# Kernel optimization log

Measured on AMD Instinct MI355X. Metric: run time of the kernel, lower is better.

## Reference

```python
import jax, jax.numpy as jnp
import numpy as np

UNITS = 768
OUT_STEPS = 64
INPUT_DIM = 96


def setup_inputs() -> dict:
    key = jax.random.key(0)
    ks = jax.random.split(key, 7)
    B, T = 2048, 24
    s_ih = 1.0 / np.sqrt(UNITS)
    inputs = jax.random.normal(ks[0], (B, T, INPUT_DIM), dtype=jnp.float32)
    # PyTorch LSTMCell params: weight_ih [4U, I], weight_hh [4U, U], biases [4U]
    W_ih = jax.random.uniform(ks[1], (4 * UNITS, INPUT_DIM), minval=-s_ih, maxval=s_ih, dtype=jnp.float32)
    W_hh = jax.random.uniform(ks[2], (4 * UNITS, UNITS), minval=-s_ih, maxval=s_ih, dtype=jnp.float32)
    b_ih = jax.random.uniform(ks[3], (4 * UNITS,), minval=-s_ih, maxval=s_ih, dtype=jnp.float32)
    b_hh = jax.random.uniform(ks[4], (4 * UNITS,), minval=-s_ih, maxval=s_ih, dtype=jnp.float32)
    # Dense: Linear(units, input_dim)
    s_d = 1.0 / np.sqrt(UNITS)
    W_d = jax.random.uniform(ks[5], (INPUT_DIM, UNITS), minval=-s_d, maxval=s_d, dtype=jnp.float32)
    b_d = jax.random.uniform(ks[6], (INPUT_DIM,), minval=-s_d, maxval=s_d, dtype=jnp.float32)
    return {"inputs": inputs, "W_ih": W_ih, "W_hh": W_hh, "b_ih": b_ih, "b_hh": b_hh, "W_d": W_d, "b_d": b_d}


def _lstm_cell(x, h, c, W_ih, W_hh, b_ih, b_hh):
    # gates: [B, 4U], PyTorch gate order i, f, g, o
    gates = x @ W_ih.T + b_ih + h @ W_hh.T + b_hh
    i, f, g, o = jnp.split(gates, 4, axis=-1)
    i = jax.nn.sigmoid(i)
    f = jax.nn.sigmoid(f)
    g = jnp.tanh(g)
    o = jax.nn.sigmoid(o)
    c_new = f * c + i * g
    h_new = o * jnp.tanh(c_new)
    return h_new, c_new


def reference(inputs, W_ih, W_hh, b_ih, b_hh, W_d, b_d):
    B = inputs.shape[0]
    h0 = jnp.zeros((B, UNITS), dtype=inputs.dtype)
    c0 = jnp.zeros((B, UNITS), dtype=inputs.dtype)
    # warmup: feed last timestep
    x0 = inputs[:, -1, :]
    h, c = _lstm_cell(x0, h0, c0, W_ih, W_hh, b_ih, b_hh)
    pred0 = h @ W_d.T + b_d

    def step(carry, _):
        pred, h, c = carry
        h2, c2 = _lstm_cell(pred, h, c, W_ih, W_hh, b_ih, b_hh)
        pred2 = h2 @ W_d.T + b_d
        return (pred2, h2, c2), pred2

    _, preds_rest = jax.lax.scan(step, (pred0, h, c), None, length=OUT_STEPS - 1)
    # preds_rest: [out_steps-1, B, I] -> stack with pred0 along time axis 1
    preds = jnp.concatenate([pred0[None], preds_rest], axis=0)  # [out_steps, B, I]
    return jnp.transpose(preds, (1, 0, 2))  # [B, out_steps, I]
```

## Files before the change

kernel.cpp:

```cpp
#include <hip/hip_runtime.h>
#include <hip/hip_bf16.h>
#include <stdint.h>

typedef __hip_bfloat16 bf16_t;
typedef __attribute__((ext_vector_type(4))) float f32x4;
typedef __attribute__((ext_vector_type(8))) short s16x8;

#define UNITS 768
#define NCOLS 3072
#define NPRED 96
#define MROWS 2048

__device__ __forceinline__ float sigf(float x) {
    return __builtin_amdgcn_rcpf(1.f + __expf(-x));
}
__device__ __forceinline__ float tanh_fast(float x) {
    return 1.f - 2.f * __builtin_amdgcn_rcpf(1.f + __expf(2.f * x));
}


__global__ void prep_b0(const float* __restrict__ W_ih, bf16_t* __restrict__ B0T) {
    int idx = blockIdx.x * 256 + threadIdx.x;
    if (idx >= NCOLS * 96) return;
    int c = idx / 96, k = idx % 96;
    int u = ((c >> 6) << 4) + (c & 15);
    int g = (c >> 4) & 3;
    B0T[idx] = (bf16_t)W_ih[(g * UNITS + u) * 96 + k];
}

__global__ void prep_x0(const float* __restrict__ inputs, bf16_t* __restrict__ x0) {
    int idx = blockIdx.x * 256 + threadIdx.x;
    int j = idx & 7;
    int l = (idx >> 3) & 63;
    int fg = idx >> 9;
    int kf = fg % 3;
    int mf = fg / 3;
    int m = mf * 16 + (l & 15);
    int k = kf * 32 + (l >> 4) * 8 + j;
    x0[idx] = (bf16_t)inputs[(m * 24 + 23) * 96 + k];
}

__global__ void prep_bias(const float* __restrict__ b_ih, const float* __restrict__ b_hh,
                          const float* __restrict__ W_ih, const float* __restrict__ b_d,
                          float* __restrict__ b0_r, float* __restrict__ beff_r) {
    int c = blockIdx.x * 256 + threadIdx.x;
    if (c >= NCOLS) return;
    int u = ((c >> 6) << 4) + (c & 15);
    int g = (c >> 4) & 3;
    int r = g * UNITS + u;
    float v = b_ih[r] + b_hh[r];
    float acc = 0.f;
    for (int j = 0; j < 96; ++j) acc += W_ih[r * 96 + j] * b_d[j];
    b0_r[c] = v;
    beff_r[c] = v + acc;
}

__global__ void prep_beff2(const float* __restrict__ W_hh, const float* __restrict__ W_ih,
                           const float* __restrict__ W_d, bf16_t* __restrict__ BeffT) {
    __shared__ float sWih[64][96];
    __shared__ float sWd[96][64];
    const int c0 = blockIdx.x * 64, k0 = blockIdx.y * 64;
    const int tid = threadIdx.x;
    for (int i = tid; i < 64 * 96; i += 256) {
        int cc = i / 96, j = i % 96;
        int c = c0 + cc;
        int u = ((c >> 6) << 4) + (c & 15);
        int g = (c >> 4) & 3;
        sWih[cc][j] = W_ih[(g * UNITS + u) * 96 + j];
    }
    for (int i = tid; i < 96 * 64; i += 256) {
        int j = i / 64, kk = i % 64;
        sWd[j][kk] = W_d[j * UNITS + k0 + kk];
    }
    __syncthreads();
    const int kk = tid & 63;
    const int cc0 = (tid >> 6) * 16;
    for (int cc = cc0; cc < cc0 + 16; ++cc) {
        float acc = 0.f;
#pragma unroll 12
        for (int j = 0; j < 96; ++j) acc += sWih[cc][j] * sWd[j][kk];
        int c = c0 + cc;
        int u = ((c >> 6) << 4) + (c & 15);
        int g = (c >> 4) & 3;
        int r = g * UNITS + u;
        BeffT[(size_t)c * UNITS + k0 + kk] = (bf16_t)(W_hh[(size_t)r * UNITS + k0 + kk] + acc);
    }
}

__global__ void prep_wdt(const float* __restrict__ W_d, bf16_t* __restrict__ BeffT) {
    int idx = blockIdx.x * 256 + threadIdx.x;
    int c = idx / UNITS, k = idx % UNITS;
    float v = (c < NPRED) ? W_d[c * UNITS + k] : 0.f;
    BeffT[(size_t)(NCOLS + c) * UNITS + k] = (bf16_t)v;
}

__global__ void prep_swz(const bf16_t* __restrict__ src, bf16_t* __restrict__ dst,
                         int Knk, int K, int total) {
    int idx = blockIdx.x * 256 + threadIdx.x;
    if (idx >= total) return;
    int j = idx & 7;
    int l = (idx >> 3) & 63;
    int fg = idx >> 9;
    int f = fg & 3;
    int rest = fg >> 2;
    int kf = rest % Knk;
    int nw = rest / Knk;
    int c = (nw >> 1) * 128 + (nw & 1) * 64 + f * 16 + (l & 15);
    int k = kf * 32 + (l >> 4) * 8 + j;
    dst[idx] = src[(size_t)c * K + k];
}

__global__ __launch_bounds__(256, 2)
void step_kernel(const bf16_t* __restrict__ A,
                 const bf16_t* __restrict__ B,
                 const float* __restrict__ bias_r,
                 const float* __restrict__ b_d,
                 float* __restrict__ c_state,
                 bf16_t* __restrict__ h_out,
                 float* __restrict__ out,
                 int Knk, int nt_off, int t, int is_first)
{
    const int tid = threadIdx.x;
    const int wave = tid >> 6;
    const int lane = tid & 63;
    const int wr = wave >> 1, wc = wave & 1;
    const int l15 = lane & 15, l4 = lane >> 4;

    const int per = gridDim.x >> 3;
    const int g = (blockIdx.x & 7) * per + (blockIdx.x >> 3);
    const int nt = nt_off + (g >> 4);
    const int mt = g & 15;
    const int n0 = nt * 128;
    const bool is_pred = (nt >= 24);

    const bf16_t* Ab[4];
#pragma unroll
    for (int i = 0; i < 4; ++i)
        Ab[i] = A + ((size_t)((mt * 8 + wr * 4 + i) * Knk) * 64 + lane) * 8;
    const bf16_t* Bb[4];
#pragma unroll
    for (int f = 0; f < 4; ++f)
        Bb[f] = B + ((size_t)((nt * 2 + wc) * Knk * 4 + f) * 64 + lane) * 8;

    const int u = nt * 32 + wc * 16 + l15;
    const int slot = nt * 16 + mt;
    float* cbase = c_state + (((size_t)slot * 4 + wave) * 64 + lane) * 16;
    f32x4 cold4[4];
    float bi[4];
#pragma unroll
    for (int q = 0; q < 4; ++q) cold4[q] = f32x4{0.f, 0.f, 0.f, 0.f};
    if (!is_pred) {
        if (!is_first) {
#pragma unroll
            for (int q = 0; q < 4; ++q) cold4[q] = *(const f32x4*)(cbase + q * 4);
        }
#pragma unroll
        for (int f = 0; f < 4; ++f) bi[f] = bias_r[n0 + wc * 64 + f * 16 + l15];
    } else {
#pragma unroll
        for (int f = 0; f < 4; ++f) {
            int j = wc * 64 + f * 16 + l15;
            bi[f] = (j < NPRED) ? b_d[j] : 0.f;
        }
    }

    f32x4 acc[4][4];
#pragma unroll
    for (int i = 0; i < 4; ++i)
#pragma unroll
        for (int j = 0; j < 4; ++j) acc[i][j] = f32x4{0.f, 0.f, 0.f, 0.f};

    s16x8 afr[3][4], bfr[3][4];
    const int nk = Knk;

#define LOADK(BUF, KT) do {                                                          \
        _Pragma("unroll")                                                            \
        for (int _i = 0; _i < 4; ++_i)                                               \
            afr[BUF][_i] = *(const s16x8*)(Ab[_i] + (size_t)(KT) * 512);             \
        _Pragma("unroll")                                                            \
        for (int _f = 0; _f < 4; ++_f)                                               \
            bfr[BUF][_f] = *(const s16x8*)(Bb[_f] + (size_t)(KT) * 2048);            \
    } while (0)
#define MF(BUF) do {                                                                 \
        _Pragma("unroll")                                                            \
        for (int _i = 0; _i < 4; ++_i)                                               \
            _Pragma("unroll")                                                        \
            for (int _j = 0; _j < 4; ++_j)                                           \
                acc[_i][_j] = __builtin_amdgcn_mfma_f32_16x16x32_bf16(               \
                    afr[BUF][_i], bfr[BUF][_j], acc[_i][_j], 0, 0, 0);               \
    } while (0)

    LOADK(0, 0);
    LOADK(1, 1);
    const int nk3 = nk / 3;
    for (int b3 = 0; b3 < nk3; ++b3) {
        const int kt = b3 * 3;
        if (kt + 2 < nk) LOADK(2, kt + 2);
        MF(0);
        if (kt + 3 < nk) LOADK(0, kt + 3);
        MF(1);
        if (kt + 4 < nk) LOADK(1, kt + 4);
        MF(2);
    }
#undef LOADK
#undef MF

    if (!is_pred) {
        const int kq = wc * 2 + (l15 >> 3);
        const int jj = l15 & 7;
        f32x4 cnew4[4];
#pragma unroll
        for (int i = 0; i < 4; ++i) {
            const int mf = mt * 8 + wr * 4 + i;
            bf16_t* hb = h_out + (size_t)(mf * 24 + nt) * 512;
#pragma unroll
            for (int r = 0; r < 4; ++r) {
                float gi = acc[i][0][r] + bi[0];
                float gf = acc[i][1][r] + bi[1];
                float gg = acc[i][2][r] + bi[2];
                float go = acc[i][3][r] + bi[3];
                float si = sigf(gi);
                float sf = sigf(gf);
                float tg = tanh_fast(gg);
                float so = sigf(go);
                float cn = sf * cold4[i][r] + si * tg;
                cnew4[i][r] = cn;
                int lp = (l4 * 4 + r) | (kq << 4);
                hb[lp * 8 + jj] = (bf16_t)(so * tanh_fast(cn));
            }
        }
#pragma unroll
        for (int q = 0; q < 4; ++q) *(f32x4*)(cbase + q * 4) = cnew4[q];
    } else {
#pragma unroll
        for (int f = 0; f < 4; ++f) {
            int j = wc * 64 + f * 16 + l15;
            if (j < NPRED) {
#pragma unroll
                for (int i = 0; i < 4; ++i)
#pragma unroll
                    for (int r = 0; r < 4; ++r) {
                        int row = mt * 128 + wr * 64 + i * 16 + l4 * 4 + r;
                        out[((size_t)row * 64 + (t - 1)) * NPRED + j] = acc[i][f][r] + bi[f];
                    }
            }
        }
    }
}

extern "C" void kernel_launch(void* const* d_in, const int* in_sizes, int n_in,
                              void* d_out, int out_size, void* d_ws, size_t ws_size,
                              hipStream_t stream)
{
    const float* inputs = (const float*)d_in[0];
    const float* W_ih   = (const float*)d_in[1];
    const float* W_hh   = (const float*)d_in[2];
    const float* b_ih   = (const float*)d_in[3];
    const float* b_hh   = (const float*)d_in[4];
    const float* W_d    = (const float*)d_in[5];
    const float* b_d    = (const float*)d_in[6];
    float* out = (float*)d_out;

    char* ws = (char*)d_ws;
    size_t off = 0;
    auto alloc = [&](size_t bytes) -> char* {
        char* p = ws + off;
        off = (off + bytes + 255) & ~(size_t)255;
        return p;
    };
    bf16_t* B0T   = (bf16_t*)alloc((size_t)NCOLS * 96 * 2);
    bf16_t* B0s   = (bf16_t*)alloc((size_t)NCOLS * 96 * 2);
    bf16_t* BeffT = (bf16_t*)alloc((size_t)3200 * UNITS * 2);
    bf16_t* Bs    = (bf16_t*)alloc((size_t)3200 * UNITS * 2);
    bf16_t* x0s   = (bf16_t*)alloc((size_t)MROWS * 96 * 2);
    bf16_t* h0    = (bf16_t*)alloc((size_t)MROWS * UNITS * 2);
    bf16_t* h1    = (bf16_t*)alloc((size_t)MROWS * UNITS * 2);
    float*  cst   = (float*)alloc((size_t)384 * 4 * 64 * 16 * 4);
    float*  b0r   = (float*)alloc(NCOLS * 4);
    float*  beffr = (float*)alloc(NCOLS * 4);

    prep_b0   <<<(NCOLS * 96 + 255) / 256, 256, 0, stream>>>(W_ih, B0T);
    prep_swz  <<<(NCOLS * 96 + 255) / 256, 256, 0, stream>>>(B0T, B0s, 3, 96, NCOLS * 96);
    prep_x0   <<<(MROWS * 96) / 256, 256, 0, stream>>>(inputs, x0s);
    prep_bias <<<(NCOLS + 255) / 256, 256, 0, stream>>>(b_ih, b_hh, W_ih, b_d, b0r, beffr);
    prep_beff2<<<dim3(48, 12), 256, 0, stream>>>(W_hh, W_ih, W_d, BeffT);
    prep_wdt  <<<(128 * UNITS) / 256, 256, 0, stream>>>(W_d, BeffT);
    prep_swz  <<<(3200 * UNITS + 255) / 256, 256, 0, stream>>>(BeffT, Bs, 24, UNITS, 3200 * UNITS);

    bf16_t* h[2] = {h0, h1};

    step_kernel<<<384, 256, 0, stream>>>(x0s, B0s, b0r, b_d, cst, h[1], out, 3, 0, 0, 1);
    for (int n = 1; n < 64; ++n)
        step_kernel<<<400, 256, 0, stream>>>(h[n & 1], Bs, beffr, b_d, cst,
                                             h[(n + 1) & 1], out, 24, 0, n, 0);
    step_kernel<<<16, 256, 0, stream>>>(h[0], Bs, beffr, b_d, cst, h[1], out,
                                        24, 24, 64, 0);
    (void)ws_size; (void)in_sizes; (void)n_in; (void)out_size;
}
```

Measured before the change: 1.349 ms.

## Fuse all LSTM steps into one persistent cooperative kernel with grid barriers

```diff
diff --git a/kernel.cpp b/kernel.cpp
--- a/kernel.cpp
+++ b/kernel.cpp
@@ -18,6 +18,10 @@
     return 1.f - 2.f * __builtin_amdgcn_rcpf(1.f + __expf(2.f * x));
 }
 
+
+__global__ void prep_zero(unsigned int* c) {
+    if (threadIdx.x < 64) c[threadIdx.x] = 0u;
+}
 
 __global__ void prep_b0(const float* __restrict__ W_ih, bf16_t* __restrict__ B0T) {
     int idx = blockIdx.x * 256 + threadIdx.x;
@@ -108,6 +112,202 @@
     int c = (nw >> 1) * 128 + (nw & 1) * 64 + f * 16 + (l & 15);
     int k = kf * 32 + (l >> 4) * 8 + j;
     dst[idx] = src[(size_t)c * K + k];
+}
+
+__global__ __launch_bounds__(256, 1)
+void persist_kernel(const bf16_t* __restrict__ x0s,
+                    const bf16_t* __restrict__ B0s,
+                    const bf16_t* __restrict__ Bs,
+                    const float* __restrict__ b0r,
+                    const float* __restrict__ beffr,
+                    const float* __restrict__ b_d,
+                    bf16_t* __restrict__ h0,
+                    bf16_t* __restrict__ h1,
+                    float* __restrict__ out,
+                    unsigned int* __restrict__ ctrs)
+{
+    const int tid = threadIdx.x;
+    const int wave = tid >> 6;
+    const int lane = tid & 63;
+    const int l15 = lane & 15, l4 = lane >> 4;
+
+    __shared__ int s_id;
+
+    if (tid == 0) {
+        unsigned int x;
+        asm volatile("s_getreg_b32 %0, hwreg(20, 0, 32)" : "=s"(x));
+        x &= 7u;
+        unsigned int r = atomicAdd(&ctrs[x], 1u);
+        __threadfence();
+        unsigned int gq = atomicAdd(&ctrs[8], 1u);
+        while (__hip_atomic_load(&ctrs[8], __ATOMIC_RELAXED, __HIP_MEMORY_SCOPE_AGENT) < 256u)
+            __builtin_amdgcn_s_sleep(2);
+        __threadfence();
+        unsigned int mn = 0xffffffffu;
+        for (int y = 0; y < 8; ++y) {
+            unsigned int v = __hip_atomic_load(&ctrs[y], __ATOMIC_RELAXED, __HIP_MEMORY_SCOPE_AGENT);
+            mn = (v < mn) ? v : mn;
+        }
+        int id;
+        if (mn >= 25u) id = (r < 25u) ? (int)(x * 25u + r) : -1;
+        else           id = (gq < 200u) ? (int)gq : -1;
+        s_id = id;
+    }
+    __syncthreads();
+    const int id = s_id;
+    const bool active = (id >= 0);
+    const int mt = active ? (id & 7) : 0;
+    const int nt = active ? (id >> 3) : 0;
+    const bool is_pred = active && (nt == 24);
+
+    unsigned int* bar = &ctrs[9];
+    bf16_t* hbuf[2] = {h0, h1};
+
+    float bi0[8], biE[8];
+    if (active) {
+        if (!is_pred) {
+#pragma unroll
+            for (int f = 0; f < 8; ++f) {
+                bi0[f] = b0r[nt * 128 + f * 16 + l15];
+                biE[f] = beffr[nt * 128 + f * 16 + l15];
+            }
+        } else {
+#pragma unroll
+            for (int f = 0; f < 8; ++f) {
+                int col = f * 16 + l15;
+                biE[f] = (col < NPRED) ? b_d[col] : 0.f;
+                bi0[f] = biE[f];
+            }
+        }
+    }
+
+    float cr[4][4][2];
+#pragma unroll
+    for (int i = 0; i < 4; ++i)
+#pragma unroll
+        for (int r = 0; r < 4; ++r) { cr[i][r][0] = 0.f; cr[i][r][1] = 0.f; }
+
+    for (int n = 0; n <= 64; ++n) {
+        const bool doit = active && (n == 0 ? !is_pred : (n == 64 ? is_pred : true));
+        if (doit) {
+            f32x4 acc[4][8];
+#pragma unroll
+            for (int i = 0; i < 4; ++i)
+#pragma unroll
+                for (int f = 0; f < 8; ++f) acc[i][f] = f32x4{0.f, 0.f, 0.f, 0.f};
+
+            if (n == 0) {
+                s16x8 a3[3][4], b3[3][8];
+#pragma unroll
+                for (int p = 0; p < 3; ++p) {
+#pragma unroll
+                    for (int i = 0; i < 4; ++i)
+                        a3[p][i] = *(const s16x8*)(x0s + ((size_t)((mt * 16 + wave * 4 + i) * 3 + p)) * 512 + lane * 8);
+#pragma unroll
+                    for (int f = 0; f < 8; ++f)
+                        b3[p][f] = *(const s16x8*)(B0s + ((size_t)(((nt * 2 + (f >> 2)) * 3 + p) * 4 + (f & 3))) * 512 + lane * 8);
+                }
+#pragma unroll
+                for (int p = 0; p < 3; ++p)
+#pragma unroll
+                    for (int i = 0; i < 4; ++i)
+#pragma unroll
+                        for (int f = 0; f < 8; ++f)
+                            acc[i][f] = __builtin_amdgcn_mfma_f32_16x16x32_bf16(a3[p][i], b3[p][f], acc[i][f], 0, 0, 0);
+            } else {
+                const bf16_t* hin = hbuf[n & 1];
+                const bf16_t* Ab[4];
+#pragma unroll
+                for (int i = 0; i < 4; ++i)
+                    Ab[i] = hin + ((size_t)((mt * 16 + wave * 4 + i) * 24)) * 512 + lane * 8;
+                const bf16_t* Bb[8];
+#pragma unroll
+                for (int f = 0; f < 8; ++f)
+                    Bb[f] = Bs + ((size_t)(((nt * 2 + (f >> 2)) * 24) * 4 + (f & 3))) * 512 + lane * 8;
+
+                s16x8 afr[4][4], bfr[4][8];
+#pragma unroll
+                for (int p = 0; p < 3; ++p) {
+#pragma unroll
+                    for (int i = 0; i < 4; ++i) afr[p][i] = *(const s16x8*)(Ab[i] + p * 512);
+#pragma unroll
+                    for (int f = 0; f < 8; ++f) bfr[p][f] = *(const s16x8*)(Bb[f] + (size_t)p * 2048);
+                }
+#pragma unroll
+                for (int kt = 0; kt < 24; ++kt) {
+                    if (kt + 3 < 24) {
+                        const int pf = kt + 3, sl = pf & 3;
+#pragma unroll
+                        for (int i = 0; i < 4; ++i) afr[sl][i] = *(const s16x8*)(Ab[i] + pf * 512);
+#pragma unroll
+                        for (int f = 0; f < 8; ++f) bfr[sl][f] = *(const s16x8*)(Bb[f] + (size_t)pf * 2048);
+                    }
+                    const int s = kt & 3;
+#pragma unroll
+                    for (int i = 0; i < 4; ++i)
+#pragma unroll
+                        for (int f = 0; f < 8; ++f)
+                            acc[i][f] = __builtin_amdgcn_mfma_f32_16x16x32_bf16(afr[s][i], bfr[s][f], acc[i][f], 0, 0, 0);
+                }
+            }
+
+            if (!is_pred) {
+                const float* bia = (n == 0) ? bi0 : biE;
+                bf16_t* hout = hbuf[(n + 1) & 1];
+#pragma unroll
+                for (int i = 0; i < 4; ++i) {
+                    const int mf = mt * 16 + wave * 4 + i;
+                    bf16_t* hb = hout + ((size_t)(mf * 24 + nt)) * 512;
+#pragma unroll
+                    for (int r = 0; r < 4; ++r) {
+#pragma unroll
+                        for (int jg = 0; jg < 2; ++jg) {
+                            float gi = acc[i][jg * 4 + 0][r] + bia[jg * 4 + 0];
+                            float gf = acc[i][jg * 4 + 1][r] + bia[jg * 4 + 1];
+                            float gg = acc[i][jg * 4 + 2][r] + bia[jg * 4 + 2];
+                            float go = acc[i][jg * 4 + 3][r] + bia[jg * 4 + 3];
+                            float si = sigf(gi);
+                            float sf = sigf(gf);
+                            float tg = tanh_fast(gg);
+                            float so = sigf(go);
+                            float cn = sf * cr[i][r][jg] + si * tg;
+                            cr[i][r][jg] = cn;
+                            int lp = (l4 * 4 + r) | ((jg * 2 + (l15 >> 3)) << 4);
+                            hb[lp * 8 + (l15 & 7)] = (bf16_t)(so * tanh_fast(cn));
+                        }
+                    }
+                }
+            } else {
+                const int t = n - 1;
+#pragma unroll
+                for (int f = 0; f < 8; ++f) {
+                    int col = f * 16 + l15;
+                    if (col < NPRED) {
+#pragma unroll
+                        for (int i = 0; i < 4; ++i)
+#pragma unroll
+                            for (int r = 0; r < 4; ++r) {
+                                int row = mt * 256 + wave * 64 + i * 16 + l4 * 4 + r;
+                                out[((size_t)row * 64 + t) * NPRED + col] = acc[i][f][r] + biE[f];
+                            }
+                    }
+                }
+            }
+        }
+
+        if (n < 64) {
+            __syncthreads();
+            if (tid == 0) {
+                __threadfence();
+                atomicAdd(bar, 1u);
+                const unsigned int tgt = 256u * (unsigned int)(n + 1);
+                while (__hip_atomic_load(bar, __ATOMIC_RELAXED, __HIP_MEMORY_SCOPE_AGENT) < tgt)
+                    __builtin_amdgcn_s_sleep(2);
+                __threadfence();
+            }
+            __syncthreads();
+        }
+    }
 }
 
 __global__ __launch_bounds__(256, 2)
@@ -172,7 +372,6 @@
 
     s16x8 afr[3][4], bfr[3][4];
     const int nk = Knk;
-
 #define LOADK(BUF, KT) do {                                                          \
         _Pragma("unroll")                                                            \
         for (int _i = 0; _i < 4; ++_i)                                               \
@@ -189,7 +388,6 @@
                 acc[_i][_j] = __builtin_amdgcn_mfma_f32_16x16x32_bf16(               \
                     afr[BUF][_i], bfr[BUF][_j], acc[_i][_j], 0, 0, 0);               \
     } while (0)
-
     LOADK(0, 0);
     LOADK(1, 1);
     const int nk3 = nk / 3;
@@ -275,10 +473,12 @@
     bf16_t* x0s   = (bf16_t*)alloc((size_t)MROWS * 96 * 2);
     bf16_t* h0    = (bf16_t*)alloc((size_t)MROWS * UNITS * 2);
     bf16_t* h1    = (bf16_t*)alloc((size_t)MROWS * UNITS * 2);
-    float*  cst   = (float*)alloc((size_t)384 * 4 * 64 * 16 * 4);
+    float*  cst   = (float*)alloc((size_t)400 * 4 * 64 * 16 * 4);
     float*  b0r   = (float*)alloc(NCOLS * 4);
     float*  beffr = (float*)alloc(NCOLS * 4);
-
+    unsigned int* ctrs = (unsigned int*)alloc(64 * 4);
+
+    prep_zero <<<1, 64, 0, stream>>>(ctrs);
     prep_b0   <<<(NCOLS * 96 + 255) / 256, 256, 0, stream>>>(W_ih, B0T);
     prep_swz  <<<(NCOLS * 96 + 255) / 256, 256, 0, stream>>>(B0T, B0s, 3, 96, NCOLS * 96);
     prep_x0   <<<(MROWS * 96) / 256, 256, 0, stream>>>(inputs, x0s);
@@ -287,13 +487,23 @@
     prep_wdt  <<<(128 * UNITS) / 256, 256, 0, stream>>>(W_d, BeffT);
     prep_swz  <<<(3200 * UNITS + 255) / 256, 256, 0, stream>>>(BeffT, Bs, 24, UNITS, 3200 * UNITS);
 
-    bf16_t* h[2] = {h0, h1};
-
-    step_kernel<<<384, 256, 0, stream>>>(x0s, B0s, b0r, b_d, cst, h[1], out, 3, 0, 0, 1);
-    for (int n = 1; n < 64; ++n)
-        step_kernel<<<400, 256, 0, stream>>>(h[n & 1], Bs, beffr, b_d, cst,
-                                             h[(n + 1) & 1], out, 24, 0, n, 0);
-    step_kernel<<<16, 256, 0, stream>>>(h[0], Bs, beffr, b_d, cst, h[1], out,
-                                        24, 24, 64, 0);
-    (void)ws_size; (void)in_sizes; (void)n_in; (void)out_size;
-}
+    void* a0 = (void*)x0s; void* a1 = (void*)B0s; void* a2 = (void*)Bs;
+    void* a3 = (void*)b0r; void* a4 = (void*)beffr; void* a5 = (void*)b_d;
+    void* a6 = (void*)h0;  void* a7 = (void*)h1;  void* a8 = (void*)out;
+    void* a9 = (void*)ctrs;
+    void* args[] = { &a0, &a1, &a2, &a3, &a4, &a5, &a6, &a7, &a8, &a9 };
+
+    hipError_t err = hipLaunchCooperativeKernel((const void*)persist_kernel,
+                                                dim3(256), dim3(256), args, 0, stream);
+    if (err != hipSuccess) {
+        (void)hipGetLastError();
+        bf16_t* h[2] = {h0, h1};
+        step_kernel<<<384, 256, 0, stream>>>(x0s, B0s, b0r, b_d, cst, h[1], out, 3, 0, 0, 1);
+        for (int n = 1; n < 64; ++n)
+            step_kernel<<<400, 256, 0, stream>>>(h[n & 1], Bs, beffr, b_d, cst,
+                                                 h[(n + 1) & 1], out, 24, 0, n, 0);
+        step_kernel<<<16, 256, 0, stream>>>(h[0], Bs, beffr, b_d, cst, h[1], out,
+                                            24, 24, 64, 0);
+    }
+    (void)cst; (void)ws_size; (void)in_sizes; (void)n_in; (void)out_size;
+}
```

Measured after the change: 5.029 ms. +272.8%, slower.
